# Kernel optimization log

Measured on AMD Instinct MI355X. Metric: run time of the kernel, lower is better.

The kernel has to match this reference:

```python
import jax, jax.numpy as jnp
import numpy as np

B, S, D, H = 4, 2048, 1024, 16
HD = D // H  # 64


def setup_inputs() -> dict:
    key = jax.random.key(0)
    ks = jax.random.split(key, 8)
    s = 0.02
    return {
        "inp_values": jax.random.normal(ks[0], (B, S, D), jnp.float32),
        "inp_keys": jax.random.normal(ks[1], (B, S, D), jnp.float32),
        "inp_queries": jax.random.normal(ks[2], (B, S, D), jnp.float32),
        # per-head projection weights, torch nn.Linear(head_dims, head_dims, bias=False): y = x @ W.T
        "Wv": jax.random.normal(ks[3], (HD, HD), jnp.float32) * s,
        "Wk": jax.random.normal(ks[4], (HD, HD), jnp.float32) * s,
        "Wq": jax.random.normal(ks[5], (HD, HD), jnp.float32) * s,
        # output projection nn.Linear(D, D) with bias
        "Wo": jax.random.normal(ks[6], (D, D), jnp.float32) * s,
        "bo": jax.random.normal(ks[7], (D,), jnp.float32) * s,
    }


def reference(inp_values, inp_keys, inp_queries, Wv, Wk, Wq, Wo, bo):
    b, sq, _ = inp_queries.shape
    sk = inp_values.shape[1]
    v = inp_values.reshape(b, sk, H, HD)
    k = inp_keys.reshape(b, sk, H, HD)
    q = inp_queries.reshape(b, sq, H, HD)
    # per-head linear: x @ W.T
    v = jnp.einsum('bshd,ed->bshe', v, Wv)
    k = jnp.einsum('bshd,ed->bshe', k, Wk)
    q = jnp.einsum('bshd,ed->bshe', q, Wq)
    # scores scaled by 1/sqrt(input_dims) as in the original (not head_dims)
    scores = jnp.einsum('bqhd,bkhd->bhqk', q, k) / jnp.sqrt(jnp.float32(D))
    attn = jax.nn.softmax(scores, axis=-1)  # [B,H,Q,K]
    out = jnp.einsum('bhqk,bkhd->bqhd', attn, v).reshape(b, sq, D)
    return out @ Wo.T + bo
```

## Files before the change

kernel.cpp:

```cpp
#include <hip/hip_runtime.h>
#include <hip/hip_bf16.h>

#define B_ 4
#define S_ 2048
#define D_ 1024
#define H_ 16
#define HD_ 64

typedef __attribute__((ext_vector_type(8))) short bf16x8;
typedef __attribute__((ext_vector_type(4))) short bf16x4;
typedef __attribute__((ext_vector_type(4))) float f32x4;

#define MFMA16(a, b, c) __builtin_amdgcn_mfma_f32_16x16x16bf16_1k(a, b, c, 0, 0, 0)

__device__ __forceinline__ float fast_exp2(float x) {
#if __has_builtin(__builtin_amdgcn_exp2f)
  return __builtin_amdgcn_exp2f(x);
#else
  return exp2f(x);
#endif
}

__device__ __forceinline__ float fast_rcp(float x) {
#if __has_builtin(__builtin_amdgcn_rcpf)
  return __builtin_amdgcn_rcpf(x);
#else
  return 1.0f / x;
#endif
}

__device__ __forceinline__ short f2bf(float x) {
  union { float f; unsigned u; } v; v.f = x;
  unsigned r = (v.u + 0x7fffu + ((v.u >> 16) & 1u)) >> 16;
  return (short)(r & 0xffffu);
}

__device__ __forceinline__ unsigned pack_trunc(float a, float b) {
  union { float f; unsigned u; } ua, ub; ua.f = a; ub.f = b;
  return (ub.u & 0xffff0000u) | (ua.u >> 16);
}

__device__ __forceinline__ void gl_lds16(const short* g, void* l) {
  __builtin_amdgcn_global_load_lds(
      (const __attribute__((address_space(1))) unsigned*)(const void*)g,
      (__attribute__((address_space(3))) unsigned*)l, 16, 0, 0);
}

__global__ __launch_bounds__(256) void wo_convert(const float* __restrict__ Wo,
                                                  short* __restrict__ wob) {
  int i = blockIdx.x * blockDim.x + threadIdx.x;
  const float4* src = (const float4*)Wo + i * 2;
  float4 a = src[0], b = src[1];
  bf16x8 o;
  o[0] = f2bf(a.x); o[1] = f2bf(a.y); o[2] = f2bf(a.z); o[3] = f2bf(a.w);
  o[4] = f2bf(b.x); o[5] = f2bf(b.y); o[6] = f2bf(b.z); o[7] = f2bf(b.w);
  ((bf16x8*)wob)[i] = o;
}

__global__ __launch_bounds__(256) void qkv_proj2(
    const float* __restrict__ inpV, const float* __restrict__ inpK,
    const float* __restrict__ inpQ, const float* __restrict__ Wv,
    const float* __restrict__ Wk, const float* __restrict__ Wq,
    short* __restrict__ vt, short* __restrict__ kp, short* __restrict__ qp) {
  __shared__ bf16x8 xbuf[1024];
  __shared__ bf16x8 wbuf[512];
  int bid = blockIdx.x;
  int t = bid >> 10;
  int bh = (bid >> 4) & 63;
  int st = bid & 15;
  int b = bh >> 4, h = bh & 15;
  int s0 = st * 128;
  int tid = threadIdx.x, wave = tid >> 6, lane = tid & 63;
  int quad = lane >> 4, l15 = lane & 15;
  const float* inp = (t == 0) ? inpV : (t == 1) ? inpK : inpQ;
  const float* W = (t == 0) ? Wv : (t == 1) ? Wk : Wq;
  float wscale = (t == 2) ? (0.03125f * 1.4426950408889634f) : 1.0f;

#pragma unroll
  for (int u = 0; u < 2; ++u) {
    int slot = tid + u * 256;
    int row = slot >> 3, g = slot & 7;
    const float4* wp = (const float4*)(W + row * 64 + g * 8);
    float4 w0 = wp[0], w1 = wp[1];
    bf16x8 o;
    o[0] = f2bf(w0.x * wscale); o[1] = f2bf(w0.y * wscale);
    o[2] = f2bf(w0.z * wscale); o[3] = f2bf(w0.w * wscale);
    o[4] = f2bf(w1.x * wscale); o[5] = f2bf(w1.y * wscale);
    o[6] = f2bf(w1.z * wscale); o[7] = f2bf(w1.w * wscale);
    wbuf[row * 8 + (g ^ (row & 7))] = o;
  }
  const float* xg = inp + (b * S_ + s0) * D_ + h * HD_;
#pragma unroll
  for (int u = 0; u < 4; ++u) {
    int slot = tid + u * 256;
    int row = slot >> 3, g = slot & 7;
    const float4* xp = (const float4*)(xg + row * D_ + g * 8);
    float4 x0 = xp[0], x1 = xp[1];
    bf16x8 o;
    o[0] = f2bf(x0.x); o[1] = f2bf(x0.y); o[2] = f2bf(x0.z); o[3] = f2bf(x0.w);
    o[4] = f2bf(x1.x); o[5] = f2bf(x1.y); o[6] = f2bf(x1.z); o[7] = f2bf(x1.w);
    xbuf[row * 8 + (g ^ (row & 7))] = o;
  }
  __syncthreads();

  if (t == 0) {
    f32x4 acc[4][2];
#pragma unroll
    for (int mt = 0; mt < 4; mt++)
#pragma unroll
      for (int nt = 0; nt < 2; nt++) { acc[mt][nt][0]=0.f; acc[mt][nt][1]=0.f; acc[mt][nt][2]=0.f; acc[mt][nt][3]=0.f; }
#pragma unroll
    for (int ks = 0; ks < 2; ++ks) {
      bf16x8 af[4], bfr[2];
#pragma unroll
      for (int mt = 0; mt < 4; ++mt) {
        int row = mt * 16 + l15;
        af[mt] = wbuf[row * 8 + ((ks * 4 + quad) ^ (row & 7))];
      }
#pragma unroll
      for (int nt = 0; nt < 2; ++nt) {
        int row = wave * 32 + nt * 16 + l15;
        bfr[nt] = xbuf[row * 8 + ((ks * 4 + quad) ^ (row & 7))];
      }
#pragma unroll
      for (int mt = 0; mt < 4; ++mt)
#pragma unroll
        for (int nt = 0; nt < 2; ++nt)
          acc[mt][nt] = __builtin_amdgcn_mfma_f32_16x16x32_bf16(
              af[mt], bfr[nt], acc[mt][nt], 0, 0, 0);
    }
    short* vb = vt + (bh * 64) * S_ + s0 + wave * 32;
#pragma unroll
    for (int mt = 0; mt < 4; ++mt)
#pragma unroll
      for (int nt = 0; nt < 2; ++nt)
#pragma unroll
        for (int r = 0; r < 4; ++r) {
          int e = mt * 16 + quad * 4 + r;
          int s = nt * 16 + l15;
          vb[e * S_ + s] = f2bf(acc[mt][nt][r]);
        }
  } else {
    f32x4 acc[2][4];
#pragma unroll
    for (int mt = 0; mt < 2; mt++)
#pragma unroll
      for (int nt = 0; nt < 4; nt++) { acc[mt][nt][0]=0.f; acc[mt][nt][1]=0.f; acc[mt][nt][2]=0.f; acc[mt][nt][3]=0.f; }
#pragma unroll
    for (int ks = 0; ks < 2; ++ks) {
      bf16x8 af[2], bfr[4];
#pragma unroll
      for (int mt = 0; mt < 2; ++mt) {
        int row = wave * 32 + mt * 16 + l15;
        af[mt] = xbuf[row * 8 + ((ks * 4 + quad) ^ (row & 7))];
      }
#pragma unroll
      for (int nt = 0; nt < 4; ++nt) {
        int row = nt * 16 + l15;
        bfr[nt] = wbuf[row * 8 + ((ks * 4 + quad) ^ (row & 7))];
      }
#pragma unroll
      for (int mt = 0; mt < 2; ++mt)
#pragma unroll
        for (int nt = 0; nt < 4; ++nt)
          acc[mt][nt] = __builtin_amdgcn_mfma_f32_16x16x32_bf16(
              af[mt], bfr[nt], acc[mt][nt], 0, 0, 0);
    }
    short* ob = ((t == 1) ? kp : qp) + (bh * S_ + s0 + wave * 32) * 64;
#pragma unroll
    for (int mt = 0; mt < 2; ++mt)
#pragma unroll
      for (int nt = 0; nt < 4; ++nt)
#pragma unroll
        for (int r = 0; r < 4; ++r) {
          int s = mt * 16 + quad * 4 + r;
          int e = nt * 16 + l15;
          ob[s * 64 + e] = f2bf(acc[mt][nt][r]);
        }
  }
}

__global__ __launch_bounds__(256) void attention(
    const short* __restrict__ qp, const short* __restrict__ kp,
    const short* __restrict__ vt, short* __restrict__ ao) {
  __shared__ bf16x8 kbuf[2][512];
  __shared__ bf16x8 vbuf[2][512];
  int bid = blockIdx.x;
  int qt = bid >> 6;
  int bh = bid & 63;
  int tid = threadIdx.x, wave = tid >> 6, lane = tid & 63;
  int quad = lane >> 4, l15 = lane & 15;

  const short* qb = qp + (bh * S_ + qt * 128 + wave * 32 + l15) * 64;
  bf16x8 bq[2][2];
  bq[0][0] = *(const bf16x8*)(qb + quad * 8);
  bq[0][1] = *(const bf16x8*)(qb + 32 + quad * 8);
  bq[1][0] = *(const bf16x8*)(qb + 1024 + quad * 8);
  bq[1][1] = *(const bf16x8*)(qb + 1024 + 32 + quad * 8);

  f32x4 o[2][4];
#pragma unroll
  for (int g = 0; g < 2; g++)
#pragma unroll
    for (int dt = 0; dt < 4; dt++) { o[g][dt][0]=0.f; o[g][dt][1]=0.f; o[g][dt][2]=0.f; o[g][dt][3]=0.f; }
  f32x4 lacc[2];
  lacc[0][0]=0.f; lacc[0][1]=0.f; lacc[0][2]=0.f; lacc[0][3]=0.f;
  lacc[1][0]=0.f; lacc[1][1]=0.f; lacc[1][2]=0.f; lacc[1][3]=0.f;

  short one_bf = (short)0x3F80;
  bf16x4 ones;
  ones[0] = (l15 == 0) ? one_bf : (short)0;
  ones[1] = ones[0]; ones[2] = ones[0]; ones[3] = ones[0];

  const short* kg = kp + bh * S_ * 64;
  const short* vg = vt + bh * 64 * S_;

  int rowA = tid >> 3, gA = (tid & 7) ^ (rowA & 7);
  int rowB = (tid + 256) >> 3, gB = (tid & 7) ^ (rowB & 7);
  const short* kA = kg + rowA * 64 + gA * 8;
  const short* kB = kg + rowB * 64 + gB * 8;
  const short* vA = vg + rowA * S_ + gA * 8;
  const short* vB = vg + rowB * S_ + gB * 8;

  gl_lds16(kA, &kbuf[0][tid]);
  gl_lds16(kB, &kbuf[0][tid + 256]);
  gl_lds16(vA, &vbuf[0][tid]);
  gl_lds16(vB, &vbuf[0][tid + 256]);

  int p = 0;
  for (int kt = 0; kt < 32; ++kt) {
    __syncthreads();
    {
      int ktn = (kt + 1) & 31;
      gl_lds16(kA + ktn * 4096, &kbuf[p ^ 1][tid]);
      gl_lds16(kB + ktn * 4096, &kbuf[p ^ 1][tid + 256]);
      gl_lds16(vA + ktn * 64, &vbuf[p ^ 1][tid]);
      gl_lds16(vB + ktn * 64, &vbuf[p ^ 1][tid + 256]);
    }

    bf16x4 pk[2][4];
#pragma unroll
    for (int nt = 0; nt < 4; ++nt) {
      int krow = nt * 16 + l15;
      bf16x8 ak0 = kbuf[p][krow * 8 + ((0 + quad) ^ (krow & 7))];
      bf16x8 ak1 = kbuf[p][krow * 8 + ((4 + quad) ^ (krow & 7))];
      f32x4 c0, c1;
      c0[0]=0.f; c0[1]=0.f; c0[2]=0.f; c0[3]=0.f;
      c1[0]=0.f; c1[1]=0.f; c1[2]=0.f; c1[3]=0.f;
      c0 = __builtin_amdgcn_mfma_f32_16x16x32_bf16(ak0, bq[0][0], c0, 0, 0, 0);
      c1 = __builtin_amdgcn_mfma_f32_16x16x32_bf16(ak0, bq[1][0], c1, 0, 0, 0);
      c0 = __builtin_amdgcn_mfma_f32_16x16x32_bf16(ak1, bq[0][1], c0, 0, 0, 0);
      c1 = __builtin_amdgcn_mfma_f32_16x16x32_bf16(ak1, bq[1][1], c1, 0, 0, 0);
      float e00 = fast_exp2(c0[0]), e01 = fast_exp2(c0[1]);
      float e02 = fast_exp2(c0[2]), e03 = fast_exp2(c0[3]);
      float e10 = fast_exp2(c1[0]), e11 = fast_exp2(c1[1]);
      float e12 = fast_exp2(c1[2]), e13 = fast_exp2(c1[3]);
      union { bf16x4 v; unsigned u[2]; } p0, p1;
      p0.u[0] = pack_trunc(e00, e01); p0.u[1] = pack_trunc(e02, e03);
      p1.u[0] = pack_trunc(e10, e11); p1.u[1] = pack_trunc(e12, e13);
      pk[0][nt] = p0.v; pk[1][nt] = p1.v;
    }
#pragma unroll
    for (int c = 0; c < 4; ++c) {
      lacc[0] = MFMA16(pk[0][c], ones, lacc[0]);
      lacc[1] = MFMA16(pk[1][c], ones, lacc[1]);
#pragma unroll
      for (int dt = 0; dt < 4; ++dt) {
        int d = dt * 16 + l15;
        int g0 = 2 * c + (quad >> 1);
        const short* vrow = (const short*)&vbuf[p][d * 8 + (g0 ^ (d & 7))];
        bf16x4 bv = *(const bf16x4*)(vrow + (quad & 1) * 4);
        o[0][dt] = MFMA16(pk[0][c], bv, o[0][dt]);
        o[1][dt] = MFMA16(pk[1][c], bv, o[1][dt]);
      }
    }
    p ^= 1;
  }

  int b = bh >> 4, h = bh & 15;
#pragma unroll
  for (int g = 0; g < 2; ++g) {
    float inv[4];
#pragma unroll
    for (int r = 0; r < 4; ++r) {
      float ls = __shfl(lacc[g][r], lane & 48, 64);
      inv[r] = fast_rcp(ls);
    }
#pragma unroll
    for (int dt = 0; dt < 4; ++dt)
#pragma unroll
      for (int r = 0; r < 4; ++r) {
        int srow = qt * 128 + wave * 32 + g * 16 + quad * 4 + r;
        ao[(b * S_ + srow) * D_ + h * 64 + dt * 16 + l15] =
            f2bf(o[g][dt][r] * inv[r]);
      }
  }
}

__global__ __launch_bounds__(256) void outproj(const short* __restrict__ A,
                                               const short* __restrict__ Bw,
                                               const float* __restrict__ bo,
                                               float* __restrict__ out) {
  __shared__ bf16x8 sa[2][1024];
  __shared__ bf16x8 sb[2][1024];
  int bid = blockIdx.x;
  int m0 = (bid >> 3) * 128, n0 = (bid & 7) * 128;
  int tid = threadIdx.x, wave = tid >> 6, lane = tid & 63;
  int quad = lane >> 4, l15 = lane & 15;
  int wm = (wave >> 1) * 64, wn = (wave & 1) * 64;
  f32x4 acc[4][4];
#pragma unroll
  for (int mt = 0; mt < 4; mt++)
#pragma unroll
    for (int nt = 0; nt < 4; nt++) { acc[mt][nt][0]=0.f; acc[mt][nt][1]=0.f; acc[mt][nt][2]=0.f; acc[mt][nt][3]=0.f; }

  const short* asrc[4];
  const short* bsrc[4];
#pragma unroll
  for (int u = 0; u < 4; ++u) {
    int slot = tid + u * 256;
    int row = slot >> 3, g = (slot & 7) ^ (row & 7);
    asrc[u] = A + (m0 + row) * 1024 + g * 8;
    bsrc[u] = Bw + (n0 + row) * 1024 + g * 8;
  }
#pragma unroll
  for (int u = 0; u < 4; ++u) {
    gl_lds16(asrc[u], &sa[0][tid + u * 256]);
    gl_lds16(bsrc[u], &sb[0][tid + u * 256]);
  }

  int p = 0;
  for (int k0 = 0; k0 < 1024; k0 += 64) {
    __syncthreads();
    int kn = (k0 + 64) & 1023;
#pragma unroll
    for (int u = 0; u < 4; ++u) {
      gl_lds16(asrc[u] + kn, &sa[p ^ 1][tid + u * 256]);
      gl_lds16(bsrc[u] + kn, &sb[p ^ 1][tid + u * 256]);
    }
#pragma unroll
    for (int ks = 0; ks < 2; ++ks) {
      bf16x8 af[4], bf[4];
#pragma unroll
      for (int mt = 0; mt < 4; ++mt) {
        int row = wm + mt * 16 + l15;
        af[mt] = sa[p][row * 8 + ((ks * 4 + quad) ^ (row & 7))];
      }
#pragma unroll
      for (int nt = 0; nt < 4; ++nt) {
        int row = wn + nt * 16 + l15;
        bf[nt] = sb[p][row * 8 + ((ks * 4 + quad) ^ (row & 7))];
      }
#pragma unroll
      for (int mt = 0; mt < 4; ++mt)
#pragma unroll
        for (int nt = 0; nt < 4; ++nt)
          acc[mt][nt] = __builtin_amdgcn_mfma_f32_16x16x32_bf16(
              af[mt], bf[nt], acc[mt][nt], 0, 0, 0);
    }
    p ^= 1;
  }
#pragma unroll
  for (int nt = 0; nt < 4; ++nt) {
    int n = n0 + wn + nt * 16 + l15;
    float bov = bo[n];
#pragma unroll
    for (int mt = 0; mt < 4; ++mt)
#pragma unroll
      for (int r = 0; r < 4; r++) {
        int m = m0 + wm + mt * 16 + quad * 4 + r;
        out[m * 1024 + n] = acc[mt][nt][r] + bov;
      }
  }
}

extern "C" void kernel_launch(void* const* d_in, const int* in_sizes, int n_in,
                              void* d_out, int out_size, void* d_ws,
                              size_t ws_size, hipStream_t stream) {
  const float* inpV = (const float*)d_in[0];
  const float* inpK = (const float*)d_in[1];
  const float* inpQ = (const float*)d_in[2];
  const float* Wv = (const float*)d_in[3];
  const float* Wk = (const float*)d_in[4];
  const float* Wq = (const float*)d_in[5];
  const float* Wo = (const float*)d_in[6];
  const float* bo = (const float*)d_in[7];
  float* out = (float*)d_out;

  char* ws = (char*)d_ws;
  short* vt = (short*)(ws);
  short* kp = (short*)(ws + (16u << 20));
  short* qp = (short*)(ws + (32u << 20));
  short* ao = (short*)(ws + (48u << 20));
  short* wob = (short*)(ws + (64u << 20));

  wo_convert<<<dim3(512), dim3(256), 0, stream>>>(Wo, wob);
  qkv_proj2<<<dim3(3072), dim3(256), 0, stream>>>(inpV, inpK, inpQ, Wv, Wk, Wq,
                                                  vt, kp, qp);
  attention<<<dim3(1024), dim3(256), 0, stream>>>(qp, kp, vt, ao);
  outproj<<<dim3(512), dim3(256), 0, stream>>>(ao, wob, bo, out);
}
```

Measured before the change: 296.5 us.

## Shrink attention tiles to 64 queries x 32 keys with 128-thread blocks

Attention blocks shrink from 256 threads handling 128 queries against 64-key tiles to 128 threads handling 64 queries against 32-key tiles. The LDS swizzle is adjusted for the narrower V tile, the grid is doubled, and launch bounds request 4 blocks per CU. The score-to-PV loops are fused so the probabilities feed the MFMAs straight away instead of being staged in a pk array, and the bf16 packing uses a single v_perm. The goal is more concurrent waves and lower register pressure, at the cost of streaming K/V from global memory twice as often and synchronising more often per unit of work.

```diff
diff --git a/kernel.cpp b/kernel.cpp
--- a/kernel.cpp
+++ b/kernel.cpp
@@ -12,6 +12,7 @@
 typedef __attribute__((ext_vector_type(4))) float f32x4;
 
 #define MFMA16(a, b, c) __builtin_amdgcn_mfma_f32_16x16x16bf16_1k(a, b, c, 0, 0, 0)
+#define MFMA32(a, b, c) __builtin_amdgcn_mfma_f32_16x16x32_bf16(a, b, c, 0, 0, 0)
 
 __device__ __forceinline__ float fast_exp2(float x) {
 #if __has_builtin(__builtin_amdgcn_exp2f)
@@ -35,9 +36,9 @@
   return (short)(r & 0xffffu);
 }
 
-__device__ __forceinline__ unsigned pack_trunc(float a, float b) {
+__device__ __forceinline__ unsigned pack_hi16(float a, float b) {
   union { float f; unsigned u; } ua, ub; ua.f = a; ub.f = b;
-  return (ub.u & 0xffff0000u) | (ua.u >> 16);
+  return __builtin_amdgcn_perm(ub.u, ua.u, 0x07060302u);
 }
 
 __device__ __forceinline__ void gl_lds16(const short* g, void* l) {
@@ -126,8 +127,7 @@
       for (int mt = 0; mt < 4; ++mt)
 #pragma unroll
         for (int nt = 0; nt < 2; ++nt)
-          acc[mt][nt] = __builtin_amdgcn_mfma_f32_16x16x32_bf16(
-              af[mt], bfr[nt], acc[mt][nt], 0, 0, 0);
+          acc[mt][nt] = MFMA32(af[mt], bfr[nt], acc[mt][nt]);
     }
     short* vb = vt + (bh * 64) * S_ + s0 + wave * 32;
 #pragma unroll
@@ -163,8 +163,7 @@
       for (int mt = 0; mt < 2; ++mt)
 #pragma unroll
         for (int nt = 0; nt < 4; ++nt)
-          acc[mt][nt] = __builtin_amdgcn_mfma_f32_16x16x32_bf16(
-              af[mt], bfr[nt], acc[mt][nt], 0, 0, 0);
+          acc[mt][nt] = MFMA32(af[mt], bfr[nt], acc[mt][nt]);
     }
     short* ob = ((t == 1) ? kp : qp) + (bh * S_ + s0 + wave * 32) * 64;
 #pragma unroll
@@ -180,32 +179,32 @@
   }
 }
 
-__global__ __launch_bounds__(256) void attention(
+__global__ __launch_bounds__(128, 4) void attention(
     const short* __restrict__ qp, const short* __restrict__ kp,
     const short* __restrict__ vt, short* __restrict__ ao) {
-  __shared__ bf16x8 kbuf[2][512];
-  __shared__ bf16x8 vbuf[2][512];
+  __shared__ bf16x8 kbuf[2][256];
+  __shared__ bf16x8 vbuf[2][256];
   int bid = blockIdx.x;
   int qt = bid >> 6;
   int bh = bid & 63;
   int tid = threadIdx.x, wave = tid >> 6, lane = tid & 63;
   int quad = lane >> 4, l15 = lane & 15;
 
-  const short* qb = qp + (bh * S_ + qt * 128 + wave * 32 + l15) * 64;
+  const short* qb = qp + (bh * S_ + qt * 64 + wave * 32 + l15) * 64;
   bf16x8 bq[2][2];
   bq[0][0] = *(const bf16x8*)(qb + quad * 8);
   bq[0][1] = *(const bf16x8*)(qb + 32 + quad * 8);
   bq[1][0] = *(const bf16x8*)(qb + 1024 + quad * 8);
   bq[1][1] = *(const bf16x8*)(qb + 1024 + 32 + quad * 8);
 
+  const f32x4 fzero = {0.f, 0.f, 0.f, 0.f};
   f32x4 o[2][4];
 #pragma unroll
   for (int g = 0; g < 2; g++)
 #pragma unroll
-    for (int dt = 0; dt < 4; dt++) { o[g][dt][0]=0.f; o[g][dt][1]=0.f; o[g][dt][2]=0.f; o[g][dt][3]=0.f; }
+    for (int dt = 0; dt < 4; dt++) o[g][dt] = fzero;
   f32x4 lacc[2];
-  lacc[0][0]=0.f; lacc[0][1]=0.f; lacc[0][2]=0.f; lacc[0][3]=0.f;
-  lacc[1][0]=0.f; lacc[1][1]=0.f; lacc[1][2]=0.f; lacc[1][3]=0.f;
+  lacc[0] = fzero; lacc[1] = fzero;
 
   short one_bf = (short)0x3F80;
   bf16x4 ones;
@@ -215,63 +214,55 @@
   const short* kg = kp + bh * S_ * 64;
   const short* vg = vt + bh * 64 * S_;
 
-  int rowA = tid >> 3, gA = (tid & 7) ^ (rowA & 7);
-  int rowB = (tid + 256) >> 3, gB = (tid & 7) ^ (rowB & 7);
-  const short* kA = kg + rowA * 64 + gA * 8;
-  const short* kB = kg + rowB * 64 + gB * 8;
-  const short* vA = vg + rowA * S_ + gA * 8;
-  const short* vB = vg + rowB * S_ + gB * 8;
+  int krow0 = tid >> 3, kg0 = (tid & 7) ^ (krow0 & 7);
+  int krow1 = (tid + 128) >> 3, kg1 = (tid & 7) ^ (krow1 & 7);
+  const short* kA = kg + krow0 * 64 + kg0 * 8;
+  const short* kB = kg + krow1 * 64 + kg1 * 8;
+  int vrow0 = tid >> 2, vg0 = (tid & 3) ^ (vrow0 & 3);
+  int vrow1 = (tid + 128) >> 2, vg1 = (tid & 3) ^ (vrow1 & 3);
+  const short* vA = vg + vrow0 * S_ + vg0 * 8;
+  const short* vB = vg + vrow1 * S_ + vg1 * 8;
 
   gl_lds16(kA, &kbuf[0][tid]);
-  gl_lds16(kB, &kbuf[0][tid + 256]);
+  gl_lds16(kB, &kbuf[0][tid + 128]);
   gl_lds16(vA, &vbuf[0][tid]);
-  gl_lds16(vB, &vbuf[0][tid + 256]);
+  gl_lds16(vB, &vbuf[0][tid + 128]);
 
   int p = 0;
-  for (int kt = 0; kt < 32; ++kt) {
+  for (int kt = 0; kt < 64; ++kt) {
     __syncthreads();
-    {
-      int ktn = (kt + 1) & 31;
-      gl_lds16(kA + ktn * 4096, &kbuf[p ^ 1][tid]);
-      gl_lds16(kB + ktn * 4096, &kbuf[p ^ 1][tid + 256]);
-      gl_lds16(vA + ktn * 64, &vbuf[p ^ 1][tid]);
-      gl_lds16(vB + ktn * 64, &vbuf[p ^ 1][tid + 256]);
-    }
-
-    bf16x4 pk[2][4];
-#pragma unroll
-    for (int nt = 0; nt < 4; ++nt) {
+    int ktn = (kt + 1) & 63;
+    gl_lds16(kA + ktn * 2048, &kbuf[p ^ 1][tid]);
+    gl_lds16(kB + ktn * 2048, &kbuf[p ^ 1][tid + 128]);
+    gl_lds16(vA + ktn * 32, &vbuf[p ^ 1][tid]);
+    gl_lds16(vB + ktn * 32, &vbuf[p ^ 1][tid + 128]);
+
+#pragma unroll
+    for (int nt = 0; nt < 2; ++nt) {
       int krow = nt * 16 + l15;
       bf16x8 ak0 = kbuf[p][krow * 8 + ((0 + quad) ^ (krow & 7))];
       bf16x8 ak1 = kbuf[p][krow * 8 + ((4 + quad) ^ (krow & 7))];
-      f32x4 c0, c1;
-      c0[0]=0.f; c0[1]=0.f; c0[2]=0.f; c0[3]=0.f;
-      c1[0]=0.f; c1[1]=0.f; c1[2]=0.f; c1[3]=0.f;
-      c0 = __builtin_amdgcn_mfma_f32_16x16x32_bf16(ak0, bq[0][0], c0, 0, 0, 0);
-      c1 = __builtin_amdgcn_mfma_f32_16x16x32_bf16(ak0, bq[1][0], c1, 0, 0, 0);
-      c0 = __builtin_amdgcn_mfma_f32_16x16x32_bf16(ak1, bq[0][1], c0, 0, 0, 0);
-      c1 = __builtin_amdgcn_mfma_f32_16x16x32_bf16(ak1, bq[1][1], c1, 0, 0, 0);
+      f32x4 c0 = MFMA32(ak0, bq[0][0], fzero);
+      f32x4 c1 = MFMA32(ak0, bq[1][0], fzero);
+      c0 = MFMA32(ak1, bq[0][1], c0);
+      c1 = MFMA32(ak1, bq[1][1], c1);
       float e00 = fast_exp2(c0[0]), e01 = fast_exp2(c0[1]);
       float e02 = fast_exp2(c0[2]), e03 = fast_exp2(c0[3]);
       float e10 = fast_exp2(c1[0]), e11 = fast_exp2(c1[1]);
       float e12 = fast_exp2(c1[2]), e13 = fast_exp2(c1[3]);
       union { bf16x4 v; unsigned u[2]; } p0, p1;
-      p0.u[0] = pack_trunc(e00, e01); p0.u[1] = pack_trunc(e02, e03);
-      p1.u[0] = pack_trunc(e10, e11); p1.u[1] = pack_trunc(e12, e13);
-      pk[0][nt] = p0.v; pk[1][nt] = p1.v;
-    }
-#pragma unroll
-    for (int c = 0; c < 4; ++c) {
-      lacc[0] = MFMA16(pk[0][c], ones, lacc[0]);
-      lacc[1] = MFMA16(pk[1][c], ones, lacc[1]);
+      p0.u[0] = pack_hi16(e00, e01); p0.u[1] = pack_hi16(e02, e03);
+      p1.u[0] = pack_hi16(e10, e11); p1.u[1] = pack_hi16(e12, e13);
+      lacc[0] = MFMA16(p0.v, ones, lacc[0]);
+      lacc[1] = MFMA16(p1.v, ones, lacc[1]);
 #pragma unroll
       for (int dt = 0; dt < 4; ++dt) {
         int d = dt * 16 + l15;
-        int g0 = 2 * c + (quad >> 1);
-        const short* vrow = (const short*)&vbuf[p][d * 8 + (g0 ^ (d & 7))];
+        int g0 = 2 * nt + (quad >> 1);
+        const short* vrow = (const short*)&vbuf[p][d * 4 + (g0 ^ (d & 3))];
         bf16x4 bv = *(const bf16x4*)(vrow + (quad & 1) * 4);
-        o[0][dt] = MFMA16(pk[0][c], bv, o[0][dt]);
-        o[1][dt] = MFMA16(pk[1][c], bv, o[1][dt]);
+        o[0][dt] = MFMA16(p0.v, bv, o[0][dt]);
+        o[1][dt] = MFMA16(p1.v, bv, o[1][dt]);
       }
     }
     p ^= 1;
@@ -290,7 +281,7 @@
     for (int dt = 0; dt < 4; ++dt)
 #pragma unroll
       for (int r = 0; r < 4; ++r) {
-        int srow = qt * 128 + wave * 32 + g * 16 + quad * 4 + r;
+        int srow = qt * 64 + wave * 32 + g * 16 + quad * 4 + r;
         ao[(b * S_ + srow) * D_ + h * 64 + dt * 16 + l15] =
             f2bf(o[g][dt][r] * inv[r]);
       }
@@ -355,8 +346,7 @@
       for (int mt = 0; mt < 4; ++mt)
 #pragma unroll
         for (int nt = 0; nt < 4; ++nt)
-          acc[mt][nt] = __builtin_amdgcn_mfma_f32_16x16x32_bf16(
-              af[mt], bf[nt], acc[mt][nt], 0, 0, 0);
+          acc[mt][nt] = MFMA32(af[mt], bf[nt], acc[mt][nt]);
     }
     p ^= 1;
   }
@@ -397,6 +387,6 @@
   wo_convert<<<dim3(512), dim3(256), 0, stream>>>(Wo, wob);
   qkv_proj2<<<dim3(3072), dim3(256), 0, stream>>>(inpV, inpK, inpQ, Wv, Wk, Wq,
                                                   vt, kp, qp);
-  attention<<<dim3(1024), dim3(256), 0, stream>>>(qp, kp, vt, ao);
+  attention<<<dim3(2048), dim3(128), 0, stream>>>(qp, kp, vt, ao);
   outproj<<<dim3(512), dim3(256), 0, stream>>>(ao, wob, bo, out);
 }
```

After: 289.0 us. 1.03x faster.
